# Kernel optimization log

Measured on AMD Instinct MI355X. Metric: run time of the kernel, lower is better.

Reference implementation:

```python
import jax, jax.numpy as jnp
import numpy as np

EMBED = 1024
HEADS = 16
HEAD_DIM = EMBED // HEADS


def setup_inputs() -> dict:
    key = jax.random.key(0)
    ks = jax.random.split(key, 8)
    N, L = 4, 2048
    values = jax.random.normal(ks[0], (N, L, EMBED), dtype=jnp.float32)
    keys_ = jax.random.normal(ks[1], (N, L, EMBED), dtype=jnp.float32)
    queries = jax.random.normal(ks[2], (N, L, EMBED), dtype=jnp.float32)
    s = 1.0 / np.sqrt(HEAD_DIM)
    Wv = jax.random.normal(ks[3], (HEAD_DIM, HEAD_DIM), dtype=jnp.float32) * s
    Wk = jax.random.normal(ks[4], (HEAD_DIM, HEAD_DIM), dtype=jnp.float32) * s
    Wq = jax.random.normal(ks[5], (HEAD_DIM, HEAD_DIM), dtype=jnp.float32) * s
    Wo = jax.random.normal(ks[6], (EMBED, EMBED), dtype=jnp.float32) * (1.0 / np.sqrt(EMBED))
    bo = jnp.zeros((EMBED,), dtype=jnp.float32)
    return {"values": values, "keys": keys_, "queries": queries,
            "Wv": Wv, "Wk": Wk, "Wq": Wq, "Wo": Wo, "bo": bo}


def reference(values, keys, queries, Wv, Wk, Wq, Wo, bo):
    N, L, _ = queries.shape
    # split heads: [N, L, H, D]
    v = values.reshape(N, -1, HEADS, HEAD_DIM)
    k = keys.reshape(N, -1, HEADS, HEAD_DIM)
    q = queries.reshape(N, L, HEADS, HEAD_DIM)
    # per-head linear (same [D,D] weight shared across heads), torch Linear: x @ W.T
    v = jnp.einsum('nlhd,ed->nlhe', v, Wv)
    k = jnp.einsum('nlhd,ed->nlhe', k, Wk)
    q = jnp.einsum('nqhd,ed->nqhe', q, Wq)
    # attention scores [N, H, Q, K], scaled by sqrt(embed_size) as in source
    scores = jnp.einsum('nqhd,nkhd->nhqk', q, k) / jnp.sqrt(jnp.float32(EMBED))
    attn = jax.nn.softmax(scores, axis=-1)
    out = jnp.einsum('nhqk,nkhd->nqhd', attn, v).reshape(N, L, EMBED)
    return out @ Wo.T + bo
```

## Files before the change

kernel.cpp:

```cpp
#include <hip/hip_runtime.h>
#include <math.h>

#define EMBED 1024
#define HEADS 16
#define HD    64
#define NB    4
#define LSEQ  2048

typedef __attribute__((ext_vector_type(8))) short bf16x8;
typedef __attribute__((ext_vector_type(16))) float f32x16;

typedef __attribute__((address_space(1))) void as1_void;
typedef __attribute__((address_space(3))) void as3_void;

__device__ __forceinline__ void gload_lds16(const void* g, void* l) {
    __builtin_amdgcn_global_load_lds((const as1_void*)g, (as3_void*)l, 16, 0, 0);
}

__device__ inline bf16x8 as_bf16x8(uint4 u) {
    union { uint4 u; bf16x8 b; } c; c.u = u; return c.b;
}
__device__ inline unsigned short bf16r(float x) {
    unsigned u = __float_as_uint(x);
    u += 0x7fffu + ((u >> 16) & 1u);
    return (unsigned short)(u >> 16);
}
__device__ inline float bfh2f(unsigned short h) {
    return __uint_as_float(((unsigned)h) << 16);
}
__device__ inline void split2(float x, float y, unsigned& hw, unsigned& lw) {
    unsigned short hx = bf16r(x), hy = bf16r(y);
    unsigned short lx = bf16r(x - bfh2f(hx)), ly = bf16r(y - bfh2f(hy));
    hw = (unsigned)hx | ((unsigned)hy << 16);
    lw = (unsigned)lx | ((unsigned)ly << 16);
}

__global__ __launch_bounds__(256, 3) void proj_kernel(
    const float* __restrict__ Xv, const float* __restrict__ Xk, const float* __restrict__ Xq,
    const float* __restrict__ Wv, const float* __restrict__ Wk, const float* __restrict__ Wq,
    unsigned short* __restrict__ Vt, unsigned short* __restrict__ Kp, unsigned short* __restrict__ Qp)
{
    __shared__ uint4 sXh[128 * 8];
    __shared__ uint4 sXl[128 * 8];
    __shared__ uint4 sWh[64 * 8];
    __shared__ uint4 sWl[64 * 8];

    const int t = threadIdx.x;
    const int lane = t & 63, w = t >> 6;
    const int l5 = lane & 31, hi = lane >> 5;
    const int h  = blockIdx.y;
    const int n  = blockIdx.x >> 4;
    const int l0 = (blockIdx.x & 15) * 128;

    const float QSC = 1.44269504088896341f / 32.0f;
    const float* Xs[3] = {Xv, Xk, Xq};
    const float* Ws[3] = {Wv, Wk, Wq};

    const int sr = t >> 1;
    const int sh = t & 1;

    for (int p = 0; p < 3; ++p) {
        __syncthreads();
        {
            const float* xb = Xs[p] + ((size_t)(n * LSEQ + l0 + sr)) * EMBED + h * HD + sh * 32;
            unsigned short* dh = (unsigned short*)sXh;
            unsigned short* dl = (unsigned short*)sXl;
            #pragma unroll
            for (int i = 0; i < 8; ++i) {
                float4 v = *(const float4*)(xb + i * 4);
                int j  = sh * 8 + i;
                int gg = j >> 1, s8 = (j & 1) * 4;
                int idx = sr * 64 + ((gg ^ (sr & 7)) * 8) + s8;
                uint2 hv, lv;
                split2(v.x, v.y, hv.x, lv.x);
                split2(v.z, v.w, hv.y, lv.y);
                *(uint2*)(dh + idx) = hv;
                *(uint2*)(dl + idx) = lv;
            }
        }
        #pragma unroll
        for (int i = 0; i < 2; ++i) {
            int u = t + 256 * i;
            int e = u >> 3, g = u & 7;
            const float* wb = Ws[p] + u * 8;
            float4 v0 = *(const float4*)(wb);
            float4 v1 = *(const float4*)(wb + 4);
            uint4 hq, lq;
            split2(v0.x, v0.y, hq.x, lq.x);
            split2(v0.z, v0.w, hq.y, lq.y);
            split2(v1.x, v1.y, hq.z, lq.z);
            split2(v1.z, v1.w, hq.w, lq.w);
            int idx = e * 8 + (g ^ (e & 7));
            sWh[idx] = hq;
            sWl[idx] = lq;
        }
        __syncthreads();

        f32x16 acc0, acc1;
        #pragma unroll
        for (int i = 0; i < 16; ++i) { acc0[i] = 0.f; acc1[i] = 0.f; }

        const int xrow = w * 32 + l5;
        const int w0r = l5, w1r = 32 + l5;
        #pragma unroll
        for (int kc = 0; kc < 4; ++kc) {
            int gsel = kc * 2 + hi;
            bf16x8 xh = as_bf16x8(sXh[xrow * 8 + (gsel ^ (xrow & 7))]);
            bf16x8 xl = as_bf16x8(sXl[xrow * 8 + (gsel ^ (xrow & 7))]);
            bf16x8 wh0 = as_bf16x8(sWh[w0r * 8 + (gsel ^ (w0r & 7))]);
            bf16x8 wl0 = as_bf16x8(sWl[w0r * 8 + (gsel ^ (w0r & 7))]);
            bf16x8 wh1 = as_bf16x8(sWh[w1r * 8 + (gsel ^ (w1r & 7))]);
            bf16x8 wl1 = as_bf16x8(sWl[w1r * 8 + (gsel ^ (w1r & 7))]);
            if (p == 0) {
                acc0 = __builtin_amdgcn_mfma_f32_32x32x16_bf16(wh0, xh, acc0, 0, 0, 0);
                acc0 = __builtin_amdgcn_mfma_f32_32x32x16_bf16(wh0, xl, acc0, 0, 0, 0);
                acc0 = __builtin_amdgcn_mfma_f32_32x32x16_bf16(wl0, xh, acc0, 0, 0, 0);
                acc1 = __builtin_amdgcn_mfma_f32_32x32x16_bf16(wh1, xh, acc1, 0, 0, 0);
                acc1 = __builtin_amdgcn_mfma_f32_32x32x16_bf16(wh1, xl, acc1, 0, 0, 0);
                acc1 = __builtin_amdgcn_mfma_f32_32x32x16_bf16(wl1, xh, acc1, 0, 0, 0);
            } else {
                acc0 = __builtin_amdgcn_mfma_f32_32x32x16_bf16(xh, wh0, acc0, 0, 0, 0);
                acc0 = __builtin_amdgcn_mfma_f32_32x32x16_bf16(xh, wl0, acc0, 0, 0, 0);
                acc0 = __builtin_amdgcn_mfma_f32_32x32x16_bf16(xl, wh0, acc0, 0, 0, 0);
                acc1 = __builtin_amdgcn_mfma_f32_32x32x16_bf16(xh, wh1, acc1, 0, 0, 0);
                acc1 = __builtin_amdgcn_mfma_f32_32x32x16_bf16(xh, wl1, acc1, 0, 0, 0);
                acc1 = __builtin_amdgcn_mfma_f32_32x32x16_bf16(xl, wh1, acc1, 0, 0, 0);
            }
        }

        if (p == 0) {
            unsigned short* vb = Vt + (((size_t)(n * HEADS + h)) * HD) * LSEQ + l0 + w * 32 + l5;
            #pragma unroll
            for (int r = 0; r < 16; ++r) {
                int er = (r & 3) + 8 * (r >> 2) + 4 * hi;
                vb[(size_t)er * LSEQ]        = bf16r(acc0[r]);
                vb[(size_t)(32 + er) * LSEQ] = bf16r(acc1[r]);
            }
        } else {
            unsigned short* dst = (p == 1) ? Kp : Qp;
            float sc = (p == 2) ? QSC : 1.0f;
            unsigned short* db = dst + (((size_t)(n * HEADS + h)) * LSEQ + l0 + w * 32) * HD;
            #pragma unroll
            for (int r = 0; r < 16; ++r) {
                int tok = (r & 3) + 8 * (r >> 2) + 4 * hi;
                db[(size_t)tok * HD + l5]      = bf16r(acc0[r] * sc);
                db[(size_t)tok * HD + 32 + l5] = bf16r(acc1[r] * sc);
            }
        }
    }
}

__global__ __launch_bounds__(256, 3) void attn_kernel(
    const unsigned short* __restrict__ Qp, const unsigned short* __restrict__ Kp,
    const unsigned short* __restrict__ Vt,
    unsigned short* __restrict__ AOh, unsigned short* __restrict__ AOl)
{
    __shared__ uint4 sK[128 * 8];
    __shared__ uint4 sV[64 * 16];
    __shared__ uint4 sP4[4 * 128];

    const int t = threadIdx.x;
    const int lane = t & 63, w = t >> 6;
    const int l5 = lane & 31, hi = lane >> 5;
    const int n = blockIdx.z, h = blockIdx.y;
    const int q0 = blockIdx.x * 128;
    const size_t hoff = ((size_t)n * HEADS + h) * (size_t)(LSEQ * HD);
    const unsigned short* Kh = Kp + hoff;
    const unsigned short* Vh = Vt + hoff;

    bf16x8 qf[4];
    {
        const uint4* qg = (const uint4*)(Qp + hoff + (size_t)(q0 + w * 32 + l5) * HD);
        #pragma unroll
        for (int kc = 0; kc < 4; ++kc) qf[kc] = as_bf16x8(qg[kc * 2 + hi]);
    }

    f32x16 Oa0, Oa1;
    #pragma unroll
    for (int i = 0; i < 16; ++i) { Oa0[i] = 0.f; Oa1[i] = 0.f; }
    float lsum = 0.f;

    uint2*       sPw = (uint2*)(sP4 + w * 128);
    const uint4* sPq = sP4 + w * 128;
    const int    psw = (l5 >> 1) & 3;

    for (int kt = 0; kt < LSEQ; kt += 128) {
        const uint4* gK = (const uint4*)(Kh + (size_t)kt * HD);
        #pragma unroll
        for (int i = 0; i < 4; ++i) {
            int u = t + 256 * i; int key = u >> 3, gd = u & 7;
            sK[key * 8 + (gd ^ (key & 7))] = gK[u];
        }
        #pragma unroll
        for (int i = 0; i < 4; ++i) {
            int u = t + 256 * i; int d = u >> 4, kg = u & 15;
            sV[d * 16 + (kg ^ (d & 7))] = *(const uint4*)(Vh + (size_t)d * LSEQ + kt + kg * 8);
        }
        __syncthreads();

        #pragma unroll
        for (int tc = 0; tc < 4; ++tc) {
            f32x16 c;
            #pragma unroll
            for (int i = 0; i < 16; ++i) c[i] = 0.f;
            int key = tc * 32 + l5;
            #pragma unroll
            for (int kc = 0; kc < 4; ++kc) {
                bf16x8 kf = as_bf16x8(sK[key * 8 + ((kc * 2 + hi) ^ (l5 & 7))]);
                c = __builtin_amdgcn_mfma_f32_32x32x16_bf16(kf, qf[kc], c, 0, 0, 0);
            }

            #pragma unroll
            for (int g = 0; g < 4; ++g) {
                float p0 = exp2f(c[4 * g]);
                float p1 = exp2f(c[4 * g + 1]);
                float p2 = exp2f(c[4 * g + 2]);
                float p3 = exp2f(c[4 * g + 3]);
                uint2 pk;
                pk.x = __builtin_amdgcn_perm(__float_as_uint(p1), __float_as_uint(p0), 0x07060302u);
                pk.y = __builtin_amdgcn_perm(__float_as_uint(p3), __float_as_uint(p2), 0x07060302u);
                lsum += (__uint_as_float(__float_as_uint(p0) & 0xffff0000u)
                       + __uint_as_float(__float_as_uint(p1) & 0xffff0000u))
                      + (__uint_as_float(__float_as_uint(p2) & 0xffff0000u)
                       + __uint_as_float(__float_as_uint(p3) & 0xffff0000u));
                sPw[l5 * 8 + ((g ^ psw) << 1) + hi] = pk;
            }

            #pragma unroll
            for (int win = 0; win < 2; ++win) {
                bf16x8 pf = as_bf16x8(sPq[l5 * 4 + (((win << 1) + hi) ^ psw)]);
                int vg = tc * 4 + (win << 1) + hi;
                bf16x8 v0 = as_bf16x8(sV[ l5       * 16 + (vg ^ (l5 & 7))]);
                Oa0 = __builtin_amdgcn_mfma_f32_32x32x16_bf16(pf, v0, Oa0, 0, 0, 0);
                bf16x8 v1 = as_bf16x8(sV[(32 + l5) * 16 + (vg ^ (l5 & 7))]);
                Oa1 = __builtin_amdgcn_mfma_f32_32x32x16_bf16(pf, v1, Oa1, 0, 0, 0);
            }
        }
        __syncthreads();
    }

    lsum += __shfl_xor(lsum, 32);
    float inv = 1.0f / lsum;
    float* sLf = (float*)sK;
    if (hi == 0) sLf[w * 32 + l5] = inv;

    unsigned short* hB = AOh + hoff;
    unsigned short* lB = AOl + hoff;
    #pragma unroll
    for (int r = 0; r < 16; ++r) {
        int qr = (r & 3) + 8 * (r >> 2) + 4 * hi;
        float invq = sLf[w * 32 + qr];
        size_t row = (size_t)(q0 + w * 32 + qr) * HD;
        float o0 = Oa0[r] * invq;
        float o1 = Oa1[r] * invq;
        unsigned short h0 = bf16r(o0), h1 = bf16r(o1);
        hB[row +      l5] = h0;
        hB[row + 32 + l5] = h1;
        lB[row +      l5] = bf16r(o0 - bfh2f(h0));
        lB[row + 32 + l5] = bf16r(o1 - bfh2f(h1));
    }
}

__global__ __launch_bounds__(256) void wsplit_kernel(
    const float* __restrict__ Wo,
    unsigned short* __restrict__ Woh, unsigned short* __restrict__ Wol)
{
    int i = blockIdx.x * 256 + threadIdx.x;
    float4 v = ((const float4*)Wo)[i];
    ushort4 h, l;
    h.x = bf16r(v.x); l.x = bf16r(v.x - bfh2f(h.x));
    h.y = bf16r(v.y); l.y = bf16r(v.y - bfh2f(h.y));
    h.z = bf16r(v.z); l.z = bf16r(v.z - bfh2f(h.z));
    h.w = bf16r(v.w); l.w = bf16r(v.w - bfh2f(h.w));
    ((ushort4*)Woh)[i] = h;
    ((ushort4*)Wol)[i] = l;
}

__global__ __launch_bounds__(256, 2) void outproj_kernel(
    const unsigned short* __restrict__ AOh, const unsigned short* __restrict__ AOl,
    const unsigned short* __restrict__ Woh, const unsigned short* __restrict__ Wol,
    const float* __restrict__ bo, float* __restrict__ out)
{
    __shared__ uint4 sAh[1024];
    __shared__ uint4 sAl[1024];
    __shared__ uint4 sBh[1024];
    __shared__ uint4 sBl[1024];

    const int t = threadIdx.x;
    const int lane = t & 63, w = t >> 6;
    const int l5 = lane & 31, hi = lane >> 5;
    const int m0 = blockIdx.x * 128;
    const int e0 = blockIdx.y * 128;
    const int n  = m0 >> 11, l0 = m0 & 2047;
    const int mr = (w & 1) * 64, nc = (w >> 1) * 64;

    f32x16 acc[2][2];
    #pragma unroll
    for (int a = 0; a < 2; ++a)
        #pragma unroll
        for (int b = 0; b < 2; ++b)
            #pragma unroll
            for (int i = 0; i < 16; ++i) acc[a][b][i] = 0.f;

    for (int hh = 0; hh < 16; ++hh) {
        const unsigned short* Ah = AOh + ((((size_t)n * HEADS + hh) * LSEQ) + l0) * HD;
        const unsigned short* Al = AOl + ((((size_t)n * HEADS + hh) * LSEQ) + l0) * HD;
        #pragma unroll
        for (int i = 0; i < 4; ++i) {
            int g = t + i * 256;
            gload_lds16(Ah + g * 8, sAh + g);
            gload_lds16(Al + g * 8, sAl + g);
            int e = g >> 3, gf = g & 7;
            size_t boff = (size_t)(e0 + e) * EMBED + hh * 64 + gf * 8;
            gload_lds16(Woh + boff, sBh + g);
            gload_lds16(Wol + boff, sBl + g);
        }
        __syncthreads();

        #pragma unroll
        for (int s = 0; s < 4; ++s) {
            int gcol = s * 2 + hi;
            bf16x8 ah0 = as_bf16x8(sAh[(mr +      l5) * 8 + gcol]);
            bf16x8 ah1 = as_bf16x8(sAh[(mr + 32 + l5) * 8 + gcol]);
            bf16x8 al0 = as_bf16x8(sAl[(mr +      l5) * 8 + gcol]);
            bf16x8 al1 = as_bf16x8(sAl[(mr + 32 + l5) * 8 + gcol]);
            bf16x8 bh0 = as_bf16x8(sBh[(nc +      l5) * 8 + gcol]);
            bf16x8 bh1 = as_bf16x8(sBh[(nc + 32 + l5) * 8 + gcol]);
            bf16x8 bl0 = as_bf16x8(sBl[(nc +      l5) * 8 + gcol]);
            bf16x8 bl1 = as_bf16x8(sBl[(nc + 32 + l5) * 8 + gcol]);

            acc[0][0] = __builtin_amdgcn_mfma_f32_32x32x16_bf16(ah0, bh0, acc[0][0], 0, 0, 0);
            acc[0][1] = __builtin_amdgcn_mfma_f32_32x32x16_bf16(ah0, bh1, acc[0][1], 0, 0, 0);
            acc[1][0] = __builtin_amdgcn_mfma_f32_32x32x16_bf16(ah1, bh0, acc[1][0], 0, 0, 0);
            acc[1][1] = __builtin_amdgcn_mfma_f32_32x32x16_bf16(ah1, bh1, acc[1][1], 0, 0, 0);

            acc[0][0] = __builtin_amdgcn_mfma_f32_32x32x16_bf16(ah0, bl0, acc[0][0], 0, 0, 0);
            acc[0][1] = __builtin_amdgcn_mfma_f32_32x32x16_bf16(ah0, bl1, acc[0][1], 0, 0, 0);
            acc[1][0] = __builtin_amdgcn_mfma_f32_32x32x16_bf16(ah1, bl0, acc[1][0], 0, 0, 0);
            acc[1][1] = __builtin_amdgcn_mfma_f32_32x32x16_bf16(ah1, bl1, acc[1][1], 0, 0, 0);

            acc[0][0] = __builtin_amdgcn_mfma_f32_32x32x16_bf16(al0, bh0, acc[0][0], 0, 0, 0);
            acc[0][1] = __builtin_amdgcn_mfma_f32_32x32x16_bf16(al0, bh1, acc[0][1], 0, 0, 0);
            acc[1][0] = __builtin_amdgcn_mfma_f32_32x32x16_bf16(al1, bh0, acc[1][0], 0, 0, 0);
            acc[1][1] = __builtin_amdgcn_mfma_f32_32x32x16_bf16(al1, bh1, acc[1][1], 0, 0, 0);
        }
        __syncthreads();
    }

    float b0 = bo[e0 + nc + l5];
    float b1 = bo[e0 + nc + 32 + l5];
    #pragma unroll
    for (int ti = 0; ti < 2; ++ti) {
        #pragma unroll
        for (int r = 0; r < 16; ++r) {
            int row = m0 + mr + ti * 32 + (r & 3) + 8 * (r >> 2) + 4 * hi;
            float* o = out + (size_t)row * EMBED + e0 + nc;
            o[l5]      = acc[ti][0][r] + b0;
            o[32 + l5] = acc[ti][1][r] + b1;
        }
    }
}

extern "C" void kernel_launch(void* const* d_in, const int* in_sizes, int n_in,
                              void* d_out, int out_size, void* d_ws, size_t ws_size,
                              hipStream_t stream)
{
    const float* values  = (const float*)d_in[0];
    const float* keys    = (const float*)d_in[1];
    const float* queries = (const float*)d_in[2];
    const float* Wv      = (const float*)d_in[3];
    const float* Wk      = (const float*)d_in[4];
    const float* Wq      = (const float*)d_in[5];
    const float* Wo      = (const float*)d_in[6];
    const float* bo      = (const float*)d_in[7];
    float* out = (float*)d_out;

    const size_t bufElems = (size_t)NB * HEADS * LSEQ * HD;
    unsigned short* Qp  = (unsigned short*)d_ws;
    unsigned short* Kp  = Qp  + bufElems;
    unsigned short* Vt  = Kp  + bufElems;
    unsigned short* AOh = Vt  + bufElems;
    unsigned short* AOl = AOh + bufElems;
    unsigned short* Woh = AOl + bufElems;
    unsigned short* Wol = Woh + (size_t)EMBED * EMBED;

    wsplit_kernel<<<dim3(1024), 256, 0, stream>>>(Wo, Woh, Wol);
    proj_kernel<<<dim3(NB * 16, HEADS), 256, 0, stream>>>(values, keys, queries, Wv, Wk, Wq, Vt, Kp, Qp);
    attn_kernel<<<dim3(LSEQ / 128, HEADS, NB), 256, 0, stream>>>(Qp, Kp, Vt, AOh, AOl);
    outproj_kernel<<<dim3(NB * LSEQ / 128, EMBED / 128), 256, 0, stream>>>(AOh, AOl, Woh, Wol, bo, out);
}
```

Measured before the change: 379.1 us.

## Keep softmax P in registers via permlane32 swap, coalesce projection loads

New measurement: 384.0 us. Within noise of the previous version (+1.3%).

```diff
diff --git a/kernel.cpp b/kernel.cpp
--- a/kernel.cpp
+++ b/kernel.cpp
@@ -56,21 +56,21 @@
     const float* Xs[3] = {Xv, Xk, Xq};
     const float* Ws[3] = {Wv, Wk, Wq};
 
-    const int sr = t >> 1;
-    const int sh = t & 1;
+    const int frow = t >> 4;
+    const int fcol = t & 15;
 
     for (int p = 0; p < 3; ++p) {
         __syncthreads();
         {
-            const float* xb = Xs[p] + ((size_t)(n * LSEQ + l0 + sr)) * EMBED + h * HD + sh * 32;
+            const float* xb = Xs[p] + ((size_t)(n * LSEQ + l0 + frow)) * EMBED + h * HD + fcol * 4;
             unsigned short* dh = (unsigned short*)sXh;
             unsigned short* dl = (unsigned short*)sXl;
             #pragma unroll
             for (int i = 0; i < 8; ++i) {
-                float4 v = *(const float4*)(xb + i * 4);
-                int j  = sh * 8 + i;
-                int gg = j >> 1, s8 = (j & 1) * 4;
-                int idx = sr * 64 + ((gg ^ (sr & 7)) * 8) + s8;
+                int row = frow + i * 16;
+                float4 v = *(const float4*)(xb + (size_t)i * 16 * EMBED);
+                int gg = fcol >> 1, s8 = (fcol & 1) * 4;
+                int idx = row * 64 + ((gg ^ (row & 7)) * 8) + s8;
                 uint2 hv, lv;
                 split2(v.x, v.y, hv.x, lv.x);
                 split2(v.z, v.w, hv.y, lv.y);
@@ -150,14 +150,13 @@
     }
 }
 
-__global__ __launch_bounds__(256, 3) void attn_kernel(
+__global__ __launch_bounds__(256, 4) void attn_kernel(
     const unsigned short* __restrict__ Qp, const unsigned short* __restrict__ Kp,
     const unsigned short* __restrict__ Vt,
     unsigned short* __restrict__ AOh, unsigned short* __restrict__ AOl)
 {
     __shared__ uint4 sK[128 * 8];
     __shared__ uint4 sV[64 * 16];
-    __shared__ uint4 sP4[4 * 128];
 
     const int t = threadIdx.x;
     const int lane = t & 63, w = t >> 6;
@@ -180,10 +179,6 @@
     for (int i = 0; i < 16; ++i) { Oa0[i] = 0.f; Oa1[i] = 0.f; }
     float lsum = 0.f;
 
-    uint2*       sPw = (uint2*)(sP4 + w * 128);
-    const uint4* sPq = sP4 + w * 128;
-    const int    psw = (l5 >> 1) & 3;
-
     for (int kt = 0; kt < LSEQ; kt += 128) {
         const uint4* gK = (const uint4*)(Kh + (size_t)kt * HD);
         #pragma unroll
@@ -210,30 +205,34 @@
                 c = __builtin_amdgcn_mfma_f32_32x32x16_bf16(kf, qf[kc], c, 0, 0, 0);
             }
 
+            unsigned pw[8];
             #pragma unroll
             for (int g = 0; g < 4; ++g) {
                 float p0 = exp2f(c[4 * g]);
                 float p1 = exp2f(c[4 * g + 1]);
                 float p2 = exp2f(c[4 * g + 2]);
                 float p3 = exp2f(c[4 * g + 3]);
-                uint2 pk;
-                pk.x = __builtin_amdgcn_perm(__float_as_uint(p1), __float_as_uint(p0), 0x07060302u);
-                pk.y = __builtin_amdgcn_perm(__float_as_uint(p3), __float_as_uint(p2), 0x07060302u);
-                lsum += (__uint_as_float(__float_as_uint(p0) & 0xffff0000u)
-                       + __uint_as_float(__float_as_uint(p1) & 0xffff0000u))
-                      + (__uint_as_float(__float_as_uint(p2) & 0xffff0000u)
-                       + __uint_as_float(__float_as_uint(p3) & 0xffff0000u));
-                sPw[l5 * 8 + ((g ^ psw) << 1) + hi] = pk;
-            }
+                lsum += (p0 + p1) + (p2 + p3);
+                asm("v_cvt_pk_bf16_f32 %0, %1, %2" : "=v"(pw[2 * g])     : "v"(p0), "v"(p1));
+                asm("v_cvt_pk_bf16_f32 %0, %1, %2" : "=v"(pw[2 * g + 1]) : "v"(p2), "v"(p3));
+            }
+            asm("v_permlane32_swap_b32 %0, %1" : "+v"(pw[0]), "+v"(pw[2]));
+            asm("v_permlane32_swap_b32 %0, %1" : "+v"(pw[1]), "+v"(pw[3]));
+            asm("v_permlane32_swap_b32 %0, %1" : "+v"(pw[4]), "+v"(pw[6]));
+            asm("v_permlane32_swap_b32 %0, %1" : "+v"(pw[5]), "+v"(pw[7]));
 
             #pragma unroll
             for (int win = 0; win < 2; ++win) {
-                bf16x8 pf = as_bf16x8(sPq[l5 * 4 + (((win << 1) + hi) ^ psw)]);
+                union { unsigned u[4]; bf16x8 b; } pf;
+                pf.u[0] = pw[4 * win];
+                pf.u[1] = pw[4 * win + 1];
+                pf.u[2] = pw[4 * win + 2];
+                pf.u[3] = pw[4 * win + 3];
                 int vg = tc * 4 + (win << 1) + hi;
                 bf16x8 v0 = as_bf16x8(sV[ l5       * 16 + (vg ^ (l5 & 7))]);
-                Oa0 = __builtin_amdgcn_mfma_f32_32x32x16_bf16(pf, v0, Oa0, 0, 0, 0);
+                Oa0 = __builtin_amdgcn_mfma_f32_32x32x16_bf16(pf.b, v0, Oa0, 0, 0, 0);
                 bf16x8 v1 = as_bf16x8(sV[(32 + l5) * 16 + (vg ^ (l5 & 7))]);
-                Oa1 = __builtin_amdgcn_mfma_f32_32x32x16_bf16(pf, v1, Oa1, 0, 0, 0);
+                Oa1 = __builtin_amdgcn_mfma_f32_32x32x16_bf16(pf.b, v1, Oa1, 0, 0, 0);
             }
         }
         __syncthreads();
```
